# Kernel tuning notes

Measured on AMD Instinct MI355X. Metric: run time of the kernel, lower is better.

The kernel has to match this reference:

```python
import jax, jax.numpy as jnp
import numpy as np

N = 50000
IN_C, HID_C, OUT_C = 128, 64, 32
E = 800000
NEG_SLOPE = 0.2


def setup_inputs() -> dict:
    key = jax.random.key(0)
    ks = jax.random.split(key, 8)
    x = jax.random.normal(ks[0], (N, IN_C), dtype=jnp.float32)
    edge_index = jax.random.randint(ks[1], (2, E), 0, N, dtype=jnp.int64)
    # GATConv params (heads=1): lin weight, att_src/att_dst vectors, bias
    sc = 1.0 / np.sqrt(IN_C)
    W = jax.random.uniform(ks[2], (IN_C, HID_C), jnp.float32, -sc, sc)
    att_src = jax.random.normal(ks[3], (HID_C,), jnp.float32) * (1.0 / np.sqrt(HID_C))
    att_dst = jax.random.normal(ks[4], (HID_C,), jnp.float32) * (1.0 / np.sqrt(HID_C))
    bias_conv = jnp.zeros((HID_C,), jnp.float32)
    sl = 1.0 / np.sqrt(HID_C)
    W_lin = jax.random.uniform(ks[5], (HID_C, OUT_C), jnp.float32, -sl, sl)
    b_lin = jax.random.uniform(ks[6], (OUT_C,), jnp.float32, -sl, sl)
    return {"x": x, "edge_index": edge_index, "W": W, "att_src": att_src,
            "att_dst": att_dst, "bias_conv": bias_conv, "W_lin": W_lin, "b_lin": b_lin}


def reference(x, edge_index, W, att_src, att_dst, bias_conv, W_lin, b_lin):
    n = x.shape[0]
    h = x @ W  # [N, HID]
    # add self-loops (PyG GATConv default add_self_loops=True)
    loop = jnp.arange(n, dtype=edge_index.dtype)
    src = jnp.concatenate([edge_index[0], loop])  # [E+N]
    dst = jnp.concatenate([edge_index[1], loop])
    a_src = h @ att_src  # [N]
    a_dst = h @ att_dst
    e = jax.nn.leaky_relu(a_src[src] + a_dst[dst], NEG_SLOPE)  # [E+N]
    # segment softmax over incoming edges per destination node
    m = jax.ops.segment_max(e, dst, num_segments=n)
    e = jnp.exp(e - m[dst])
    denom = jax.ops.segment_sum(e, dst, num_segments=n)
    alpha = e / (denom[dst] + 1e-16)
    msg = alpha[:, None] * h[src]  # [E+N, HID]
    out = jax.ops.segment_sum(msg, dst, num_segments=n) + bias_conv
    out = jax.nn.relu(out)
    return out @ W_lin + b_lin
```

## Files before the change

### kernel.cpp

```cpp
#include <hip/hip_runtime.h>
#include <hip/hip_bf16.h>

#define IN_C  128
#define HID_C 64
#define OUT_C 32
#define NEG_SLOPE 0.2f
#define EPB1    2048
#define BUCKETW 64
#define RCAP    1536
#define NBKT    1024
#define CSTRIDE 16
#define XS_LD   136

typedef short bf16x8 __attribute__((ext_vector_type(8)));
typedef float f32x4  __attribute__((ext_vector_type(4)));

__device__ __forceinline__ unsigned short f2bf(float f) {
    __hip_bfloat16 h = __float2bfloat16(f);
    return *(unsigned short*)&h;
}
__device__ __forceinline__ float bflo(unsigned int u) {
    return __uint_as_float(u << 16);
}
__device__ __forceinline__ float bfhi(unsigned int u) {
    return __uint_as_float(u & 0xffff0000u);
}

__global__ __launch_bounds__(256) void gemm_bin1_kernel(
    const float* __restrict__ x, const float* __restrict__ W,
    const float* __restrict__ att_src, const float* __restrict__ att_dst,
    __hip_bfloat16* __restrict__ hb,
    float* __restrict__ a_src, float* __restrict__ a_dst,
    const int* __restrict__ ei, int E,
    int* __restrict__ bcur, unsigned* __restrict__ bucketbuf,
    int ngemm, int n_nodes)
{
    __shared__ __align__(16) unsigned char smem[34816];
    const int t = threadIdx.x;

    if ((int)blockIdx.x < ngemm) {
        unsigned short* xs = (unsigned short*)smem;
        unsigned short* wt = (unsigned short*)(smem + 17408);
        const int wv   = t >> 6;
        const int lane = t & 63;
        const int m16  = lane & 15;
        const int quad = lane >> 4;
        const int node0 = blockIdx.x * 64;
        const int nrows = min(64, n_nodes - node0);

        {
            const float4* xg = (const float4*)(x + (long)node0 * IN_C);
#pragma unroll
            for (int i = t; i < 2048; i += 256) {
                const int row = i >> 5;
                const int c4  = i & 31;
                float4 v = (row < nrows) ? xg[i] : make_float4(0.f, 0.f, 0.f, 0.f);
                ushort4 u;
                u.x = f2bf(v.x); u.y = f2bf(v.y);
                u.z = f2bf(v.z); u.w = f2bf(v.w);
                *(ushort4*)(xs + row * XS_LD + c4 * 4) = u;
            }
        }
        {
#pragma unroll
            for (int i = t; i < 2048; i += 256) {
                const int k  = i >> 4;
                const int n0 = (i & 15) * 4;
                const float4 v = *(const float4*)(W + k * HID_C + n0);
                wt[(n0 + 0) * XS_LD + k] = f2bf(v.x);
                wt[(n0 + 1) * XS_LD + k] = f2bf(v.y);
                wt[(n0 + 2) * XS_LD + k] = f2bf(v.z);
                wt[(n0 + 3) * XS_LD + k] = f2bf(v.w);
            }
        }
        __syncthreads();

        const int myrow0 = wv * 16;
        bf16x8 A[4];
#pragma unroll
        for (int k0 = 0; k0 < 4; ++k0)
            A[k0] = *(const bf16x8*)(xs + (myrow0 + m16) * XS_LD + k0 * 32 + quad * 8);

        f32x4 C[4];
#pragma unroll
        for (int c = 0; c < 4; ++c) {
            C[c] = (f32x4){0.f, 0.f, 0.f, 0.f};
#pragma unroll
            for (int k0 = 0; k0 < 4; ++k0) {
                const bf16x8 B = *(const bf16x8*)(wt + (c * 16 + m16) * XS_LD + k0 * 32 + quad * 8);
                C[c] = __builtin_amdgcn_mfma_f32_16x16x32_bf16(A[k0], B, C[c], 0, 0, 0);
            }
        }

#pragma unroll
        for (int c = 0; c < 4; ++c) {
#pragma unroll
            for (int r = 0; r < 4; ++r) {
                const int row = myrow0 + quad * 4 + r;
                if (row < nrows)
                    hb[(long)(node0 + row) * HID_C + c * 16 + m16] = __float2bfloat16(C[c][r]);
            }
        }

        {
            float ps[4] = {0.f, 0.f, 0.f, 0.f};
            float pd[4] = {0.f, 0.f, 0.f, 0.f};
#pragma unroll
            for (int c = 0; c < 4; ++c) {
                const float av = att_src[c * 16 + m16];
                const float dv = att_dst[c * 16 + m16];
#pragma unroll
                for (int r = 0; r < 4; ++r) {
                    ps[r] = fmaf(C[c][r], av, ps[r]);
                    pd[r] = fmaf(C[c][r], dv, pd[r]);
                }
            }
#pragma unroll
            for (int off = 1; off <= 8; off <<= 1) {
#pragma unroll
                for (int r = 0; r < 4; ++r) {
                    ps[r] += __shfl_xor(ps[r], off, 64);
                    pd[r] += __shfl_xor(pd[r], off, 64);
                }
            }
            if (m16 == 0) {
#pragma unroll
                for (int r = 0; r < 4; ++r) {
                    const int row = myrow0 + quad * 4 + r;
                    if (row < nrows) {
                        a_src[node0 + row] = ps[r];
                        a_dst[node0 + row] = pd[r];
                    }
                }
            }
        }
    } else {
        unsigned* stage = (unsigned*)smem;
        int* excl = (int*)(smem + 8192);
        int* cur  = (int*)(smem + 12288);
        int* gpos = (int*)(smem + 16384);
        int* wsum = (int*)(smem + 20480);

        const int base = (blockIdx.x - ngemm) * EPB1;
        const int nedge = min(EPB1, E - base);
        const int lane = t & 63, wv = t >> 6;

        for (int i = t; i < NBKT; i += 256) excl[i] = 0;
        __syncthreads();

        for (int i = t; i < nedge; i += 256)
            atomicAdd(&excl[ei[E + base + i] >> 6], 1);
        __syncthreads();

        {
            const int b0 = t * 4;
            const int c0 = excl[b0], c1 = excl[b0 + 1], c2 = excl[b0 + 2], c3 = excl[b0 + 3];
            const int tsum = c0 + c1 + c2 + c3;
            int incl = tsum;
#pragma unroll
            for (int off = 1; off <= 32; off <<= 1) {
                int u = __shfl_up(incl, off, 64);
                if (lane >= off) incl += u;
            }
            if (lane == 63) wsum[wv] = incl;
            __syncthreads();
            int wbase = 0;
#pragma unroll
            for (int w = 0; w < 4; ++w) wbase += (w < wv) ? wsum[w] : 0;
            int run = wbase + (incl - tsum);
            excl[b0]     = run; cur[b0]     = run; run += c0;
            excl[b0 + 1] = run; cur[b0 + 1] = run; run += c1;
            excl[b0 + 2] = run; cur[b0 + 2] = run; run += c2;
            excl[b0 + 3] = run; cur[b0 + 3] = run;
        }
        __syncthreads();

        for (int i = t; i < nedge; i += 256) {
            const int s = ei[base + i];
            const int d = ei[E + base + i];
            const int b = d >> 6;
            const int pos = atomicAdd(&cur[b], 1);
            stage[pos] = (unsigned)s | ((unsigned)(d & 63) << 16)
                         | ((unsigned)b << 22);
        }
        __syncthreads();

        for (int b = t; b < NBKT; b += 256) {
            const int c = cur[b] - excl[b];
            gpos[b] = (c > 0) ? atomicAdd(&bcur[b * CSTRIDE], c) : 0;
        }
        __syncthreads();

        for (int i = t; i < nedge; i += 256) {
            const unsigned r = stage[i];
            const int b = r >> 22;
            const int dp = gpos[b] + (i - excl[b]);
            if (dp < RCAP) bucketbuf[(long)b * RCAP + dp] = r & 0x3FFFFFu;
        }
    }
}

__global__ __launch_bounds__(512) void bucket_agg_kernel(
    const unsigned* __restrict__ bucketbuf, const int* __restrict__ bcursor,
    const __hip_bfloat16* __restrict__ hb,
    const float* __restrict__ a_src, const float* __restrict__ a_dst,
    const float* __restrict__ bias_conv,
    const float* __restrict__ W_lin, const float* __restrict__ b_lin,
    float* __restrict__ out, int n_nodes)
{
    __shared__ unsigned srtL[RCAP];
    __shared__ int cntd[BUCKETW];
    __shared__ int rp[BUCKETW + 1];
    __shared__ int curd[BUCKETW];

    const int t  = threadIdx.x;
    const int q  = blockIdx.x;
    const int d0 = q * BUCKETW;
    const int dmax = min(BUCKETW, n_nodes - d0);
    const int tot  = min(bcursor[q * CSTRIDE], RCAP);
    const int wv = t >> 6, lane = t & 63, g8 = lane >> 3, l = lane & 7;

    if (t < BUCKETW) cntd[t] = 0;
    __syncthreads();

    const unsigned* gsrc = bucketbuf + (long)q * RCAP;

    for (int i = t; i < tot; i += 512)
        atomicAdd(&cntd[(gsrc[i] >> 16) & 63], 1);
    __syncthreads();

    if (t < 64) {
        int c = cntd[t], incl = c;
#pragma unroll
        for (int off = 1; off <= 32; off <<= 1) {
            int u = __shfl_up(incl, off, 64);
            if (t >= off) incl += u;
        }
        rp[t] = incl - c;
        curd[t] = incl - c;
        if (t == 63) rp[64] = incl;
    }
    __syncthreads();

    for (int i = t; i < tot; i += 512) {
        const unsigned r = gsrc[i];
        const int pos = atomicAdd(&curd[(r >> 16) & 63], 1);
        srtL[pos] = r;
    }
    __syncthreads();

    float Wr[8][4];
#pragma unroll
    for (int kc = 0; kc < 8; ++kc)
#pragma unroll
        for (int kj = 0; kj < 4; ++kj)
            Wr[kc][kj] = W_lin[(l * 8 + kc) * OUT_C + g8 * 4 + kj];
    float biasR[8];
#pragma unroll
    for (int kc = 0; kc < 8; ++kc) biasR[kc] = bias_conv[l * 8 + kc];
    float blinR[4];
#pragma unroll
    for (int kj = 0; kj < 4; ++kj) blinR[kj] = b_lin[g8 * 4 + kj];

    const unsigned short* hbs = (const unsigned short*)hb;

    for (int dloc = wv; dloc < dmax; dloc += 8) {
        const int d = d0 + dloc;
        const float ad = a_dst[d];
        float A[8] = {0.f,0.f,0.f,0.f,0.f,0.f,0.f,0.f};
        float den = 0.f;
        if (g8 == 0) {
            float e = a_src[d] + ad;
            e = (e >= 0.f) ? e : NEG_SLOPE * e;
            const float ws = __expf(e);
            const uint4 hv = *(const uint4*)(hbs + (long)d * HID_C + l * 8);
            den = ws;
            A[0] = ws * bflo(hv.x); A[1] = ws * bfhi(hv.x);
            A[2] = ws * bflo(hv.y); A[3] = ws * bfhi(hv.y);
            A[4] = ws * bflo(hv.z); A[5] = ws * bfhi(hv.z);
            A[6] = ws * bflo(hv.w); A[7] = ws * bfhi(hv.w);
        }
        const int beg = rp[dloc], fin = rp[dloc + 1];
        for (int j = beg + g8; j < fin; j += 16) {
            const int  j1   = j + 8;
            const bool has1 = j1 < fin;
            const unsigned r0 = srtL[j];
            const unsigned r1 = srtL[has1 ? j1 : j];
            const int   s0 = r0 & 0xFFFF;
            const int   s1 = r1 & 0xFFFF;
            const float as0 = a_src[s0];
            const float as1 = a_src[s1];
            const uint4 h0 = *(const uint4*)(hbs + (long)s0 * HID_C + l * 8);
            const uint4 h1 = *(const uint4*)(hbs + (long)s1 * HID_C + l * 8);
            float e0 = as0 + ad; e0 = (e0 >= 0.f) ? e0 : NEG_SLOPE * e0;
            float e1 = as1 + ad; e1 = (e1 >= 0.f) ? e1 : NEG_SLOPE * e1;
            const float w0 = __expf(e0);
            const float w1 = has1 ? __expf(e1) : 0.f;
            den += w0 + w1;
            A[0] = fmaf(w0, bflo(h0.x), A[0]); A[1] = fmaf(w0, bfhi(h0.x), A[1]);
            A[2] = fmaf(w0, bflo(h0.y), A[2]); A[3] = fmaf(w0, bfhi(h0.y), A[3]);
            A[4] = fmaf(w0, bflo(h0.z), A[4]); A[5] = fmaf(w0, bfhi(h0.z), A[5]);
            A[6] = fmaf(w0, bflo(h0.w), A[6]); A[7] = fmaf(w0, bfhi(h0.w), A[7]);
            A[0] = fmaf(w1, bflo(h1.x), A[0]); A[1] = fmaf(w1, bfhi(h1.x), A[1]);
            A[2] = fmaf(w1, bflo(h1.y), A[2]); A[3] = fmaf(w1, bfhi(h1.y), A[3]);
            A[4] = fmaf(w1, bflo(h1.z), A[4]); A[5] = fmaf(w1, bfhi(h1.z), A[5]);
            A[6] = fmaf(w1, bflo(h1.w), A[6]); A[7] = fmaf(w1, bfhi(h1.w), A[7]);
        }
#pragma unroll
        for (int off = 8; off <= 32; off <<= 1) {
#pragma unroll
            for (int k = 0; k < 8; ++k) A[k] += __shfl_xor(A[k], off, 64);
            den += __shfl_xor(den, off, 64);
        }
        const float rd = 1.0f / (den + 1e-16f);
        float p0 = 0.f, p1 = 0.f, p2 = 0.f, p3 = 0.f;
#pragma unroll
        for (int kc = 0; kc < 8; ++kc) {
            float vv = fmaf(A[kc], rd, biasR[kc]);
            vv = vv > 0.f ? vv : 0.f;
            p0 = fmaf(vv, Wr[kc][0], p0);
            p1 = fmaf(vv, Wr[kc][1], p1);
            p2 = fmaf(vv, Wr[kc][2], p2);
            p3 = fmaf(vv, Wr[kc][3], p3);
        }
#pragma unroll
        for (int off = 1; off <= 4; off <<= 1) {
            p0 += __shfl_xor(p0, off, 64);
            p1 += __shfl_xor(p1, off, 64);
            p2 += __shfl_xor(p2, off, 64);
            p3 += __shfl_xor(p3, off, 64);
        }
        if (l == 0) {
            float4 o = make_float4(p0 + blinR[0], p1 + blinR[1],
                                   p2 + blinR[2], p3 + blinR[3]);
            *(float4*)(out + (long)d * OUT_C + g8 * 4) = o;
        }
    }
}

extern "C" void kernel_launch(void* const* d_in, const int* in_sizes, int n_in,
                              void* d_out, int out_size, void* d_ws, size_t ws_size,
                              hipStream_t stream) {
    const float* x         = (const float*)d_in[0];
    const int*   ei        = (const int*)d_in[1];
    const float* W         = (const float*)d_in[2];
    const float* att_src   = (const float*)d_in[3];
    const float* att_dst   = (const float*)d_in[4];
    const float* bias_conv = (const float*)d_in[5];
    const float* W_lin     = (const float*)d_in[6];
    const float* b_lin     = (const float*)d_in[7];
    float*       out       = (float*)d_out;

    const int n_nodes = in_sizes[0] / IN_C;
    const int E       = in_sizes[1] / 2;
    const int B1   = (E + EPB1 - 1) / EPB1;
    const int Q    = (n_nodes + BUCKETW - 1) / BUCKETW;
    const int NG   = (n_nodes + 63) / 64;

    __hip_bfloat16* hb = (__hip_bfloat16*)d_ws;
    float* a_src   = (float*)(hb + (long)n_nodes * HID_C);
    float* a_dst   = a_src + n_nodes;
    int*   bcur    = (int*)(a_dst + n_nodes);
    unsigned* bucketbuf = (unsigned*)(bcur + (long)Q * CSTRIDE);

    hipMemsetAsync(bcur, 0, (size_t)Q * CSTRIDE * sizeof(int), stream);

    gemm_bin1_kernel<<<NG + B1, 256, 0, stream>>>(
        x, W, att_src, att_dst, hb, a_src, a_dst,
        ei, E, bcur, bucketbuf, NG, n_nodes);

    bucket_agg_kernel<<<Q, 512, 0, stream>>>(
        bucketbuf, bcur, hb, a_src, a_dst,
        bias_conv, W_lin, b_lin, out, n_nodes);
}
```

Before: 161.5 us.

## Double block size in GEMM/binning kernel, stage h stores via LDS, register-cache bucket loads

```diff
diff --git a/kernel.cpp b/kernel.cpp
--- a/kernel.cpp
+++ b/kernel.cpp
@@ -5,7 +5,7 @@
 #define HID_C 64
 #define OUT_C 32
 #define NEG_SLOPE 0.2f
-#define EPB1    2048
+#define EPB1    4096
 #define BUCKETW 64
 #define RCAP    1536
 #define NBKT    1024
@@ -26,7 +26,7 @@
     return __uint_as_float(u & 0xffff0000u);
 }
 
-__global__ __launch_bounds__(256) void gemm_bin1_kernel(
+__global__ __launch_bounds__(512) void gemm_bin1_kernel(
     const float* __restrict__ x, const float* __restrict__ W,
     const float* __restrict__ att_src, const float* __restrict__ att_dst,
     __hip_bfloat16* __restrict__ hb,
@@ -35,23 +35,23 @@
     int* __restrict__ bcur, unsigned* __restrict__ bucketbuf,
     int ngemm, int n_nodes)
 {
-    __shared__ __align__(16) unsigned char smem[34816];
+    __shared__ __align__(16) unsigned char smem[52224];
     const int t = threadIdx.x;
 
     if ((int)blockIdx.x < ngemm) {
         unsigned short* xs = (unsigned short*)smem;
-        unsigned short* wt = (unsigned short*)(smem + 17408);
+        unsigned short* wt = (unsigned short*)(smem + 34816);
         const int wv   = t >> 6;
         const int lane = t & 63;
         const int m16  = lane & 15;
         const int quad = lane >> 4;
-        const int node0 = blockIdx.x * 64;
-        const int nrows = min(64, n_nodes - node0);
+        const int node0 = blockIdx.x * 128;
+        const int nrows = min(128, n_nodes - node0);
 
         {
             const float4* xg = (const float4*)(x + (long)node0 * IN_C);
 #pragma unroll
-            for (int i = t; i < 2048; i += 256) {
+            for (int i = t; i < 4096; i += 512) {
                 const int row = i >> 5;
                 const int c4  = i & 31;
                 float4 v = (row < nrows) ? xg[i] : make_float4(0.f, 0.f, 0.f, 0.f);
@@ -63,7 +63,7 @@
         }
         {
 #pragma unroll
-            for (int i = t; i < 2048; i += 256) {
+            for (int i = t; i < 2048; i += 512) {
                 const int k  = i >> 4;
                 const int n0 = (i & 15) * 4;
                 const float4 v = *(const float4*)(W + k * HID_C + n0);
@@ -95,11 +95,8 @@
 #pragma unroll
         for (int c = 0; c < 4; ++c) {
 #pragma unroll
-            for (int r = 0; r < 4; ++r) {
-                const int row = myrow0 + quad * 4 + r;
-                if (row < nrows)
-                    hb[(long)(node0 + row) * HID_C + c * 16 + m16] = __float2bfloat16(C[c][r]);
-            }
+            for (int r = 0; r < 4; ++r)
+                xs[(myrow0 + quad * 4 + r) * XS_LD + c * 16 + m16] = f2bf(C[c][r]);
         }
 
         {
@@ -134,28 +131,41 @@
                 }
             }
         }
+        __syncthreads();
+
+        {
+#pragma unroll
+            for (int i = t; i < 1024; i += 512) {
+                const int row = i >> 3;
+                const int c8  = (i & 7) * 8;
+                if (row < nrows) {
+                    const uint4 v = *(const uint4*)(xs + row * XS_LD + c8);
+                    *(uint4*)((unsigned short*)hb + (long)(node0 + row) * HID_C + c8) = v;
+                }
+            }
+        }
     } else {
         unsigned* stage = (unsigned*)smem;
-        int* excl = (int*)(smem + 8192);
-        int* cur  = (int*)(smem + 12288);
-        int* gpos = (int*)(smem + 16384);
-        int* wsum = (int*)(smem + 20480);
+        int* excl = (int*)(smem + 16384);
+        int* cur  = (int*)(smem + 20480);
+        int* gpos = (int*)(smem + 24576);
+        int* wsum = (int*)(smem + 28672);
 
         const int base = (blockIdx.x - ngemm) * EPB1;
         const int nedge = min(EPB1, E - base);
         const int lane = t & 63, wv = t >> 6;
 
-        for (int i = t; i < NBKT; i += 256) excl[i] = 0;
-        __syncthreads();
-
-        for (int i = t; i < nedge; i += 256)
+        for (int i = t; i < NBKT; i += 512) excl[i] = 0;
+        __syncthreads();
+
+        for (int i = t; i < nedge; i += 512)
             atomicAdd(&excl[ei[E + base + i] >> 6], 1);
         __syncthreads();
 
         {
-            const int b0 = t * 4;
-            const int c0 = excl[b0], c1 = excl[b0 + 1], c2 = excl[b0 + 2], c3 = excl[b0 + 3];
-            const int tsum = c0 + c1 + c2 + c3;
+            const int b0 = t * 2;
+            const int c0 = excl[b0], c1 = excl[b0 + 1];
+            const int tsum = c0 + c1;
             int incl = tsum;
 #pragma unroll
             for (int off = 1; off <= 32; off <<= 1) {
@@ -166,16 +176,14 @@
             __syncthreads();
             int wbase = 0;
 #pragma unroll
-            for (int w = 0; w < 4; ++w) wbase += (w < wv) ? wsum[w] : 0;
+            for (int w = 0; w < 8; ++w) wbase += (w < wv) ? wsum[w] : 0;
             int run = wbase + (incl - tsum);
             excl[b0]     = run; cur[b0]     = run; run += c0;
-            excl[b0 + 1] = run; cur[b0 + 1] = run; run += c1;
-            excl[b0 + 2] = run; cur[b0 + 2] = run; run += c2;
-            excl[b0 + 3] = run; cur[b0 + 3] = run;
-        }
-        __syncthreads();
-
-        for (int i = t; i < nedge; i += 256) {
+            excl[b0 + 1] = run; cur[b0 + 1] = run;
+        }
+        __syncthreads();
+
+        for (int i = t; i < nedge; i += 512) {
             const int s = ei[base + i];
             const int d = ei[E + base + i];
             const int b = d >> 6;
@@ -185,13 +193,13 @@
         }
         __syncthreads();
 
-        for (int b = t; b < NBKT; b += 256) {
+        for (int b = t; b < NBKT; b += 512) {
             const int c = cur[b] - excl[b];
             gpos[b] = (c > 0) ? atomicAdd(&bcur[b * CSTRIDE], c) : 0;
         }
         __syncthreads();
 
-        for (int i = t; i < nedge; i += 256) {
+        for (int i = t; i < nedge; i += 512) {
             const unsigned r = stage[i];
             const int b = r >> 22;
             const int dp = gpos[b] + (i - excl[b]);
@@ -225,8 +233,15 @@
 
     const unsigned* gsrc = bucketbuf + (long)q * RCAP;
 
-    for (int i = t; i < tot; i += 512)
-        atomicAdd(&cntd[(gsrc[i] >> 16) & 63], 1);
+    const int i0 = t, i1 = t + 512, i2 = t + 1024;
+    const bool v0 = i0 < tot, v1 = i1 < tot, v2 = i2 < tot;
+    const unsigned rr0 = v0 ? gsrc[i0] : 0u;
+    const unsigned rr1 = v1 ? gsrc[i1] : 0u;
+    const unsigned rr2 = v2 ? gsrc[i2] : 0u;
+
+    if (v0) atomicAdd(&cntd[(rr0 >> 16) & 63], 1);
+    if (v1) atomicAdd(&cntd[(rr1 >> 16) & 63], 1);
+    if (v2) atomicAdd(&cntd[(rr2 >> 16) & 63], 1);
     __syncthreads();
 
     if (t < 64) {
@@ -242,11 +257,9 @@
     }
     __syncthreads();
 
-    for (int i = t; i < tot; i += 512) {
-        const unsigned r = gsrc[i];
-        const int pos = atomicAdd(&curd[(r >> 16) & 63], 1);
-        srtL[pos] = r;
-    }
+    if (v0) { const int pos = atomicAdd(&curd[(rr0 >> 16) & 63], 1); srtL[pos] = rr0; }
+    if (v1) { const int pos = atomicAdd(&curd[(rr1 >> 16) & 63], 1); srtL[pos] = rr1; }
+    if (v2) { const int pos = atomicAdd(&curd[(rr2 >> 16) & 63], 1); srtL[pos] = rr2; }
     __syncthreads();
 
     float Wr[8][4];
@@ -355,7 +368,7 @@
     const int E       = in_sizes[1] / 2;
     const int B1   = (E + EPB1 - 1) / EPB1;
     const int Q    = (n_nodes + BUCKETW - 1) / BUCKETW;
-    const int NG   = (n_nodes + 63) / 64;
+    const int NG   = (n_nodes + 127) / 128;
 
     __hip_bfloat16* hb = (__hip_bfloat16*)d_ws;
     float* a_src   = (float*)(hb + (long)n_nodes * HID_C);
@@ -365,7 +378,7 @@
 
     hipMemsetAsync(bcur, 0, (size_t)Q * CSTRIDE * sizeof(int), stream);
 
-    gemm_bin1_kernel<<<NG + B1, 256, 0, stream>>>(
+    gemm_bin1_kernel<<<NG + B1, 512, 0, stream>>>(
         x, W, att_src, att_dst, hb, a_src, a_dst,
         ei, E, bcur, bucketbuf, NG, n_nodes);
 
```

Result: faster. 150.5 us (-6.8%).
